# Optimization experiments

Hardware: AMD Instinct MI355X
Metric: run time of the kernel (lower is better)

The kernel has to match this reference:

```python
import jax, jax.numpy as jnp
import numpy as np

B, D, E, H, A = 4096, 1024, 8, 1024, 512  # batch, state_dim, num_options, num_neurons, num_actions


def setup_inputs() -> dict:
    key = jax.random.key(0)
    ks = jax.random.split(key, 16)
    s = 0.02
    return {
        "state": jax.random.normal(ks[0], (B, D), jnp.float32),
        "selected_options": jax.random.randint(ks[1], (B,), 0, E, jnp.int32),
        # option network: Linear(D,H) -> ReLU -> Linear(H,E)
        "Wo1": jax.random.normal(ks[2], (D, H), jnp.float32) * s,
        "bo1": jnp.zeros((H,), jnp.float32),
        "Wo2": jax.random.normal(ks[3], (H, E), jnp.float32) * s,
        "bo2": jnp.zeros((E,), jnp.float32),
        # E expert nets, each: Linear(D,H)+ReLU -> Linear(H,H)+ReLU -> Linear(H,A)
        "We1": jax.random.normal(ks[4], (E, D, H), jnp.float32) * s,
        "be1": jnp.zeros((E, H), jnp.float32),
        "We2": jax.random.normal(ks[5], (E, H, H), jnp.float32) * s,
        "be2": jnp.zeros((E, H), jnp.float32),
        "We3": jax.random.normal(ks[6], (E, H, A), jnp.float32) * s,
        "be3": jnp.zeros((E, A), jnp.float32),
        # termination network: Linear(D,H) -> ReLU -> Linear(H,1) -> Sigmoid
        "Wt1": jax.random.normal(ks[7], (D, H), jnp.float32) * s,
        "bt1": jnp.zeros((H,), jnp.float32),
        "Wt2": jax.random.normal(ks[8], (H, 1), jnp.float32) * s,
        "bt2": jnp.zeros((1,), jnp.float32),
    }


def reference(state, selected_options, Wo1, bo1, Wo2, bo2,
              We1, be1, We2, be2, We3, be3, Wt1, bt1, Wt2, bt2):
    # option head
    option_probs = jax.nn.softmax(jnp.maximum(state @ Wo1 + bo1, 0.0) @ Wo2 + bo2, axis=-1)

    # expert MLPs: compute all experts vectorized, then gather per-sample selected expert.
    # (the torch code loops per sample; equal action sizes so no padding is needed)
    h = jnp.maximum(jnp.einsum("bd,edh->beh", state, We1) + be1, 0.0)   # [B,E,H]
    h = jnp.maximum(jnp.einsum("beh,ehk->bek", h, We2) + be2, 0.0)      # [B,E,H]
    logits = jnp.einsum("beh,eha->bea", h, We3) + be3                   # [B,E,A]
    probs_all = jax.nn.softmax(logits, axis=-1)
    sel = selected_options[:, None, None]
    action_probs = jnp.take_along_axis(probs_all, sel, axis=1)[:, 0, :]  # [B,A]
    selected_actions = jnp.argmax(action_probs, axis=-1)

    # termination head
    termination_prob = jax.nn.sigmoid(jnp.maximum(state @ Wt1 + bt1, 0.0) @ Wt2 + bt2)

    return option_probs, action_probs, termination_prob, selected_options, selected_actions
```

## Files before the change

kernel.cpp:

```cpp
#include <hip/hip_runtime.h>
#include <hip/hip_bf16.h>

#define B_ 4096
#define D_ 1024
#define E_ 8
#define H_ 1024
#define A_ 512
#define PB 6144
#define NTT 24
#define FB_CAP 128
#define FROWS (E_ * FB_CAP)
#define KSPLIT 4
#define MARGIN 3.0e-3f

typedef __attribute__((ext_vector_type(8))) short s16x8;
typedef __attribute__((ext_vector_type(4))) float f32x4;

__device__ __forceinline__ unsigned short f2bf(float f) {
    __hip_bfloat16 h = __float2bfloat16(f);
    return *reinterpret_cast<unsigned short*>(&h);
}
__device__ __forceinline__ float bf2f(unsigned short u) {
    return __uint_as_float(((unsigned int)u) << 16);
}
__device__ __forceinline__ void gload16(const void* g, void* l) {
    __builtin_amdgcn_global_load_lds(
        (const __attribute__((address_space(1))) unsigned int*)g,
        (__attribute__((address_space(3))) unsigned int*)l, 16, 0, 0);
}

__device__ __forceinline__ int a_src_chunk(int lane) { return (((lane & 7) ^ (lane >> 3)) * 8); }

__device__ __forceinline__ int t32idx(int k, int c2) {
    return k * 64 + ((c2 + 5 * (k >> 3) + k) & 63);
}

__device__ __forceinline__ void tr_tile_128x128(const float* __restrict__ src, int Nsrc,
                                                unsigned short* __restrict__ dst,
                                                unsigned int* T32) {
    const int t = threadIdx.x;
#pragma unroll
    for (int i = 0; i < 16; ++i) {
        const int id = t + i * 256;
        const int r  = id >> 5;
        const int c4 = (id & 31) * 4;
        const float4 v = *(const float4*)&src[(size_t)r * Nsrc + c4];
        const unsigned int u0 = (unsigned)f2bf(v.x) | ((unsigned)f2bf(v.y) << 16);
        const unsigned int u1 = (unsigned)f2bf(v.z) | ((unsigned)f2bf(v.w) << 16);
        T32[t32idx(r, (c4 >> 1) + 0)] = u0;
        T32[t32idx(r, (c4 >> 1) + 1)] = u1;
    }
    __syncthreads();
#pragma unroll
    for (int q = 0; q < 8; ++q) {
        const int id = t + q * 256;
        const int n = id >> 4;
        const int L = id & 15;
        const int hi = n & 1;
        unsigned int w[4];
#pragma unroll
        for (int jj = 0; jj < 4; ++jj) {
            const int k0 = L * 8 + 2 * jj;
            const unsigned int a = T32[t32idx(k0,     n >> 1)];
            const unsigned int b = T32[t32idx(k0 + 1, n >> 1)];
            const unsigned int ha = hi ? (a >> 16) : (a & 0xffffu);
            const unsigned int hb = hi ? (b >> 16) : (b & 0xffffu);
            w[jj] = ha | (hb << 16);
        }
        *(uint4*)&dst[(size_t)n * 1024 + L * 8] = make_uint4(w[0], w[1], w[2], w[3]);
    }
}

__global__ __launch_bounds__(256)
void k_prep(const float* __restrict__ x, unsigned short* __restrict__ y,
            const float* __restrict__ Wo1, const float* __restrict__ Wt1,
            unsigned short* __restrict__ Wbf,
            const float* __restrict__ We1, unsigned short* __restrict__ We1t,
            const float* __restrict__ We2, unsigned short* __restrict__ We2t,
            const float* __restrict__ We3, unsigned short* __restrict__ We3t,
            const int* __restrict__ sel, int* __restrict__ tile_expert,
            int* __restrict__ rowlist, int* __restrict__ pos_of_row,
            int* __restrict__ rowlist2, int* __restrict__ cur2) {
    __shared__ unsigned int T32[128 * 64];
    const int t = threadIdx.x;
    const int bid = blockIdx.x;
    if (bid >= 2177) {
        const int q = bid - 2177;
        const int e = q >> 5, r = q & 31, kt = r >> 2, ntb = r & 3;
        tr_tile_128x128(We3 + (size_t)e * 524288 + (size_t)(kt * 128) * 512 + ntb * 128, 512,
                        We3t + (size_t)e * 524288 + (size_t)(ntb * 128) * 1024 + kt * 128, T32);
        return;
    }
    if (bid >= 1665) {
        const int q = bid - 1665;
        const int e = q >> 6, r = q & 63, kt = r >> 3, ntb = r & 7;
        tr_tile_128x128(We2 + (size_t)e * 1048576 + (size_t)(kt * 128) * 1024 + ntb * 128, 1024,
                        We2t + (size_t)e * 1048576 + (size_t)(ntb * 128) * 1024 + kt * 128, T32);
        return;
    }
    if (bid >= 1153) {
        const int q = bid - 1153;
        const int e = q >> 6, r = q & 63, kt = r >> 3, ntb = r & 7;
        tr_tile_128x128(We1 + (size_t)e * 1048576 + (size_t)(kt * 128) * 1024 + ntb * 128, 1024,
                        We1t + (size_t)e * 1048576 + (size_t)(ntb * 128) * 1024 + kt * 128, T32);
        return;
    }
    if (bid >= 1025) {
        const int q = bid - 1025;
        const int m = q >> 6, r = q & 63, kt = r >> 3, ntb = r & 7;
        const float* src = (m ? Wt1 : Wo1) + (size_t)(kt * 128) * 1024 + ntb * 128;
        tr_tile_128x128(src, 1024,
                        Wbf + (size_t)(m * 1024 + ntb * 128) * 1024 + kt * 128, T32);
        return;
    }
    if (bid > 0) {
        const int base = (bid - 1) * 1024 + t;
#pragma unroll
        for (int j = 0; j < 4; ++j) {
            const int i = base + j * 256;
            float4 v = ((const float4*)x)[i];
            ushort4 o;
            o.x = f2bf(v.x); o.y = f2bf(v.y); o.z = f2bf(v.z); o.w = f2bf(v.w);
            ((ushort4*)y)[i] = o;
        }
        return;
    }
    __shared__ int scnt[E_], soff[E_], scur[E_];
    if (t < E_) { scnt[t] = 0; scur[t] = 0; cur2[t] = 0; }
    for (int i = t; i < PB; i += 256) rowlist[i] = -1;
    for (int i = t; i < FROWS; i += 256) rowlist2[i] = -1;
    __syncthreads();
    for (int b = t; b < B_; b += 256) {
        int e = sel[b]; e = e < 0 ? 0 : (e >= E_ ? E_ - 1 : e);
        atomicAdd(&scnt[e], 1);
    }
    __syncthreads();
    if (t == 0) {
        int off = 0;
        for (int e = 0; e < E_; ++e) {
            soff[e] = off;
            int tiles = (scnt[e] + 255) >> 8;
            for (int k = 0; k < tiles; ++k) tile_expert[(off >> 8) + k] = e;
            off += tiles << 8;
        }
        for (int k = off >> 8; k < NTT; ++k) tile_expert[k] = -1;
    }
    __syncthreads();
    for (int b = t; b < B_; b += 256) {
        int e = sel[b]; e = e < 0 ? 0 : (e >= E_ ? E_ - 1 : e);
        int pos = atomicAdd(&scur[e], 1);
        int p = soff[e] + pos; if (p >= PB) p = PB - 1;
        rowlist[p] = b;
        pos_of_row[b] = p;
    }
}

template<int TN>
__device__ __forceinline__ void gemm3(
    const unsigned short* __restrict__ g0, const unsigned short* __restrict__ g1,
    const unsigned short* __restrict__ g2, const unsigned short* __restrict__ g3,
    const unsigned short* __restrict__ Bt, int Kg, const float* __restrict__ bp,
    unsigned short* __restrict__ Cbf, float* __restrict__ Cf, int Ncols, int relu,
    unsigned short* As, unsigned short* Bs)
{
    constexpr int NI = TN / 32;
    constexpr int BTH = TN * 64;
    constexpr int BR = TN / 64;
    constexpr int LPT = 4 + BR;
    const int t = threadIdx.x, lane = t & 63, w = t >> 6;
    const int wr = w >> 1, wc = w & 1;
    const int aseg = w * 2048 + lane * 8;
    const int bseg = w * (BR * 512) + lane * 8;
    const int coffb = a_src_chunk(lane);
    const unsigned short* bsrc = Bt + (size_t)(w * BR * 8 + (lane >> 3)) * Kg + coffb;

    f32x4 acc[4][NI];
#pragma unroll
    for (int i = 0; i < 4; ++i)
#pragma unroll
        for (int j = 0; j < NI; ++j)
#pragma unroll
            for (int r = 0; r < 4; ++r) acc[i][j][r] = 0.f;

#define G_STAGE(IT, BUF) {                                                   \
        const int ko_ = (IT) * 64;                                           \
        const int oa_ = (BUF) * 16384 + aseg;                                \
        gload16(g0 + ko_, As + oa_);                                         \
        gload16(g1 + ko_, As + oa_ + 512);                                   \
        gload16(g2 + ko_, As + oa_ + 1024);                                  \
        gload16(g3 + ko_, As + oa_ + 1536);                                  \
        const int ob_ = (BUF) * BTH + bseg;                                  \
        _Pragma("unroll")                                                    \
        for (int j_ = 0; j_ < BR; ++j_)                                      \
            gload16(bsrc + ko_ + (size_t)(j_ * 8) * Kg, Bs + ob_ + j_ * 512); \
    }

    G_STAGE(0, 0);

    for (int it = 0; it < 16; ++it) {
        const int cb = it & 1;
        if (it + 1 < 16) {
            G_STAGE(it + 1, cb ^ 1);
            if constexpr (LPT == 8)      asm volatile("s_waitcnt vmcnt(8)" ::: "memory");
            else if constexpr (LPT == 6) asm volatile("s_waitcnt vmcnt(6)" ::: "memory");
            else                         asm volatile("s_waitcnt vmcnt(5)" ::: "memory");
        } else {
            asm volatile("s_waitcnt vmcnt(0)" ::: "memory");
        }
        __builtin_amdgcn_s_barrier();
        __builtin_amdgcn_sched_barrier(0);
        __builtin_amdgcn_s_setprio(1);
#pragma unroll
        for (int kq = 0; kq < 2; ++kq) {
            const int sc = kq * 4 + (lane >> 4);
            s16x8 af[4], bfr[NI];
#pragma unroll
            for (int mi = 0; mi < 4; ++mi) {
                const int ar = wr * 64 + mi * 16 + (lane & 15);
                af[mi] = *reinterpret_cast<const s16x8*>(
                    &As[cb * 16384 + ar * 64 + ((sc ^ (ar & 7)) << 3)]);
            }
#pragma unroll
            for (int ni = 0; ni < NI; ++ni) {
                const int br = wc * (TN / 2) + ni * 16 + (lane & 15);
                bfr[ni] = *reinterpret_cast<const s16x8*>(
                    &Bs[cb * BTH + br * 64 + ((sc ^ (br & 7)) << 3)]);
            }
#pragma unroll
            for (int mi = 0; mi < 4; ++mi)
#pragma unroll
                for (int ni = 0; ni < NI; ++ni)
                    acc[mi][ni] = __builtin_amdgcn_mfma_f32_16x16x32_bf16(
                        af[mi], bfr[ni], acc[mi][ni], 0, 0, 0);
        }
        __builtin_amdgcn_s_setprio(0);
        if (it + 1 < 16) {
            asm volatile("s_waitcnt lgkmcnt(0)" ::: "memory");
            __builtin_amdgcn_sched_barrier(0);
            __builtin_amdgcn_s_barrier();
        }
    }
#undef G_STAGE

    const int cq = lane >> 4, cr = lane & 15;
#pragma unroll
    for (int ni = 0; ni < NI; ++ni) {
        const int col_l = wc * (TN / 2) + ni * 16 + cr;
        const float bv = bp[col_l];
#pragma unroll
        for (int mi = 0; mi < 4; ++mi) {
#pragma unroll
            for (int r = 0; r < 4; ++r) {
                const int row_l = wr * 64 + mi * 16 + cq * 4 + r;
                float v = acc[mi][ni][r] + bv;
                if (relu) v = fmaxf(v, 0.f);
                const size_t idx = (size_t)row_l * Ncols + col_l;
                if (Cbf) Cbf[idx] = f2bf(v);
                if (Cf)  Cf[idx] = v;
            }
        }
    }
}

__global__ __launch_bounds__(512, 2)
void k_d2(const unsigned short* __restrict__ Sbf,
          const int* __restrict__ rowlist, const int* __restrict__ tile_expert,
          const unsigned short* __restrict__ Wbf,
          const float* __restrict__ bo1, const float* __restrict__ bt1,
          const unsigned short* __restrict__ We1t, const float* __restrict__ be1,
          unsigned short* __restrict__ hopt, unsigned short* __restrict__ hterm,
          unsigned short* __restrict__ h1) {
    __shared__ __align__(16) unsigned short SMEM[4 * 16384];
    unsigned short* As = SMEM;
    unsigned short* Bs = SMEM + 2 * 16384;
    const int bid = blockIdx.x;
    const int t = threadIdx.x, lane = t & 63, w = t >> 6;
    const int coff = a_src_chunk(lane);
    const int r0l = w * 32 + (lane >> 3);
    if (bid < 128) {
        const int nt = bid & 7, mt = bid >> 3;
        const unsigned short* g0 = Sbf + (size_t)(mt * 256 + r0l) * D_ + coff;
        const unsigned short* g1 = g0 + (size_t)8 * D_;
        const unsigned short* g2 = g0 + (size_t)16 * D_;
        const unsigned short* g3 = g0 + (size_t)24 * D_;
        int ntRow; const float* bp; unsigned short* C;
        if (nt < 4) { ntRow = nt * 256; bp = bo1 + nt * 256;
                      C = hopt + (size_t)(mt * 256) * H_ + nt * 256; }
        else { ntRow = 1024 + (nt - 4) * 256; bp = bt1 + (nt - 4) * 256;
               C = hterm + (size_t)(mt * 256) * H_ + (nt - 4) * 256; }
        gemm3<256>(g0, g1, g2, g3, Wbf + (size_t)ntRow * 1024, 1024, bp,
                   C, nullptr, H_, 1, As, Bs);
    } else {
        const int q = bid - 128, nt = q & 3, mt = q >> 2;
        const int e = tile_expert[mt]; if (e < 0) return;
        const int base = mt * 256;
        const int sub = rowlist[base]; if (sub < 0) return;
        int r0 = rowlist[base + r0l];      if (r0 < 0) r0 = sub;
        int r1 = rowlist[base + r0l + 8];  if (r1 < 0) r1 = sub;
        int r2 = rowlist[base + r0l + 16]; if (r2 < 0) r2 = sub;
        int r3 = rowlist[base + r0l + 24]; if (r3 < 0) r3 = sub;
        const unsigned short* g0 = Sbf + (size_t)r0 * D_ + coff;
        const unsigned short* g1 = Sbf + (size_t)r1 * D_ + coff;
        const unsigned short* g2 = Sbf + (size_t)r2 * D_ + coff;
        const unsigned short* g3 = Sbf + (size_t)r3 * D_ + coff;
        gemm3<256>(g0, g1, g2, g3,
                   We1t + (size_t)e * 1048576 + (size_t)(nt * 256) * 1024, 1024,
                   be1 + (size_t)e * H_ + nt * 256,
                   h1 + (size_t)(mt * 256) * H_ + nt * 256, nullptr, H_, 1, As, Bs);
    }
}

__global__ __launch_bounds__(512, 2)
void k_d3(const unsigned short* __restrict__ h1, const int* __restrict__ tile_expert,
          const unsigned short* __restrict__ We2t, const float* __restrict__ be2,
          unsigned short* __restrict__ h2) {
    __shared__ __align__(16) unsigned short SMEM[2 * 16384 + 2 * 8192];
    unsigned short* As = SMEM;
    unsigned short* Bs = SMEM + 2 * 16384;
    const int t = threadIdx.x, lane = t & 63, w = t >> 6;
    const int coff = a_src_chunk(lane);
    const int r0l = w * 32 + (lane >> 3);
    const int nt = blockIdx.x & 7, mt = blockIdx.x >> 3;
    const int e = tile_expert[mt]; if (e < 0) return;
    const unsigned short* g0 = h1 + (size_t)(mt * 256 + r0l) * H_ + coff;
    gemm3<128>(g0, g0 + (size_t)8 * H_, g0 + (size_t)16 * H_, g0 + (size_t)24 * H_,
               We2t + (size_t)e * 1048576 + (size_t)(nt * 128) * 1024, 1024,
               be2 + (size_t)e * H_ + nt * 128,
               h2 + (size_t)(mt * 256) * H_ + nt * 128, nullptr, H_, 1, As, Bs);
}

__global__ __launch_bounds__(512, 2)
void k_d5(const unsigned short* __restrict__ h2, const int* __restrict__ tile_expert,
          const unsigned short* __restrict__ We3t, const float* __restrict__ be3,
          float* __restrict__ lgt) {
    __shared__ __align__(16) unsigned short SMEM[2 * 16384 + 2 * 4096];
    unsigned short* As = SMEM;
    unsigned short* Bs = SMEM + 2 * 16384;
    const int t = threadIdx.x, lane = t & 63, w = t >> 6;
    const int coff = a_src_chunk(lane);
    const int r0l = w * 32 + (lane >> 3);
    const int nt = blockIdx.x & 7, mt = blockIdx.x >> 3;
    const int e = tile_expert[mt]; if (e < 0) return;
    const unsigned short* g0 = h2 + (size_t)(mt * 256 + r0l) * H_ + coff;
    gemm3<64>(g0, g0 + (size_t)8 * H_, g0 + (size_t)16 * H_, g0 + (size_t)24 * H_,
              We3t + (size_t)e * 524288 + (size_t)(nt * 64) * 1024, 1024,
              be3 + (size_t)e * A_ + nt * 64,
              nullptr, lgt + (size_t)(mt * 256) * A_ + nt * 64, A_, 0, As, Bs);
}

__device__ __forceinline__ void opt_body(int b, const unsigned short* __restrict__ h,
                                         const float* __restrict__ Wo2, const float* __restrict__ bo2,
                                         float* __restrict__ out, float* sm) {
    const int t = threadIdx.x;
    float acc[E_];
#pragma unroll
    for (int j = 0; j < E_; ++j) acc[j] = 0.f;
    for (int k = t; k < H_; k += 256) {
        float hv = bf2f(h[(size_t)b * H_ + k]);
#pragma unroll
        for (int j = 0; j < E_; ++j) acc[j] = fmaf(hv, Wo2[k * E_ + j], acc[j]);
    }
#pragma unroll
    for (int j = 0; j < E_; ++j)
        for (int off = 32; off; off >>= 1) acc[j] += __shfl_down(acc[j], off, 64);
    float* red = sm;
    float* probs = sm + 4 * E_;
    int wave = t >> 6, lane = t & 63;
    if (lane == 0)
        for (int j = 0; j < E_; ++j) red[wave * E_ + j] = acc[j];
    __syncthreads();
    if (t == 0) {
        float z[E_]; float m = -1e30f;
        for (int j = 0; j < E_; ++j) {
            z[j] = red[j] + red[E_ + j] + red[2 * E_ + j] + red[3 * E_ + j] + bo2[j];
            m = fmaxf(m, z[j]);
        }
        float s = 0.f;
        for (int j = 0; j < E_; ++j) { z[j] = expf(z[j] - m); s += z[j]; }
        float inv = 1.f / s;
        for (int j = 0; j < E_; ++j) probs[j] = z[j] * inv;
    }
    __syncthreads();
    if (t < E_) out[(size_t)b * E_ + t] = probs[t];
}

__device__ __forceinline__ void term_body(int b, const unsigned short* __restrict__ h,
                                          const float* __restrict__ Wt2, const float* __restrict__ bt2,
                                          float* __restrict__ out, float* sm) {
    const int t = threadIdx.x;
    float acc = 0.f;
    for (int k = t; k < H_; k += 256) acc = fmaf(bf2f(h[(size_t)b * H_ + k]), Wt2[k], acc);
    for (int off = 32; off; off >>= 1) acc += __shfl_down(acc, off, 64);
    if ((t & 63) == 0) sm[t >> 6] = acc;
    __syncthreads();
    if (t == 0) {
        float z = sm[0] + sm[1] + sm[2] + sm[3] + bt2[0];
        out[b] = 1.f / (1.f + expf(-z));
    }
}

__global__ __launch_bounds__(256)
void k_gather(const float* __restrict__ logits, const int* __restrict__ pos_of_row,
              const int* __restrict__ sel,
              float* __restrict__ out_probs, float* __restrict__ out_selopt,
              float* __restrict__ out_selact,
              int* __restrict__ rowlist2, int* __restrict__ cur2,
              const unsigned short* __restrict__ hopt, const float* __restrict__ Wo2,
              const float* __restrict__ bo2, float* __restrict__ out_opt,
              const unsigned short* __restrict__ hterm, const float* __restrict__ Wt2,
              const float* __restrict__ bt2, float* __restrict__ out_term) {
    __shared__ float smbuf[5 * E_ + 8];
    const int bid = blockIdx.x;
    if (bid >= 2 * B_) { term_body(bid - 2 * B_, hterm, Wt2, bt2, out_term, smbuf); return; }
    if (bid >= B_)     { opt_body(bid - B_, hopt, Wo2, bo2, out_opt, smbuf); return; }

    const int b = bid;
    int p = pos_of_row[b];
    if (p < 0) p = 0; if (p >= PB) p = PB - 1;
    const int t = threadIdx.x;
    const float* L = logits + (size_t)p * A_;
    float v0 = L[t], v1 = L[t + 256];

    float bv; int bi;
    if (v0 >= v1) { bv = v0; bi = t; } else { bv = v1; bi = t + 256; }
    for (int off = 32; off; off >>= 1) {
        float ov = __shfl_down(bv, off, 64);
        int   oi = __shfl_down(bi, off, 64);
        if (ov > bv || (ov == bv && oi < bi)) { bv = ov; bi = oi; }
    }
    __shared__ float rv[4]; __shared__ int ri[4];
    int wave = t >> 6, lane = t & 63;
    if (lane == 0) { rv[wave] = bv; ri[wave] = bi; }
    __syncthreads();
    __shared__ float sM; __shared__ int sBi;
    if (t == 0) {
        float mv = rv[0]; int mi = ri[0];
        for (int w = 1; w < 4; ++w)
            if (rv[w] > mv || (rv[w] == mv && ri[w] < mi)) { mv = rv[w]; mi = ri[w]; }
        sM = mv; sBi = mi;
    }
    __syncthreads();
    const float M = sM; const int BI = sBi;

    float e0 = expf(v0 - M), e1 = expf(v1 - M);
    float s = e0 + e1;
    for (int off = 32; off; off >>= 1) s += __shfl_down(s, off, 64);
    __shared__ float reds[4];
    if (lane == 0) reds[wave] = s;
    __syncthreads();
    float inv = 1.f / (reds[0] + reds[1] + reds[2] + reds[3]);

    out_probs[(size_t)b * A_ + t]       = e0 * inv;
    out_probs[(size_t)b * A_ + t + 256] = e1 * inv;

    float s0 = (t == BI) ? -1e30f : v0;
    float s1 = (t + 256 == BI) ? -1e30f : v1;
    float sm = fmaxf(s0, s1);
    for (int off = 32; off; off >>= 1) sm = fmaxf(sm, __shfl_down(sm, off, 64));
    __shared__ float red2[4];
    if (lane == 0) red2[wave] = sm;
    __syncthreads();

    if (t == 0) {
        float second = fmaxf(fmaxf(red2[0], red2[1]), fmaxf(red2[2], red2[3]));
        out_selact[b] = (float)BI;
        int e = sel[b]; e = e < 0 ? 0 : (e >= E_ ? E_ - 1 : e);
        out_selopt[b] = (float)sel[b];
        if (M - second < MARGIN) {
            int pos = atomicAdd(&cur2[e], 1);
            if (pos < FB_CAP) rowlist2[e * FB_CAP + pos] = b;
        }
    }
}

#define BM 64
#define BN 64
#define BK 32

__global__ __launch_bounds__(256)
void k_pgemm(const float* __restrict__ A, int lda, const int* __restrict__ flags,
             int gather, const float* __restrict__ W,
             float* __restrict__ P, int K, int N) {
    __shared__ float As_[BK][BM + 4];
    __shared__ float Bs_[BK][BN];

    const int mt = blockIdx.y, nt = blockIdx.x, kz = blockIdx.z;
    if (flags[mt * BM] < 0) return;
    const int e = mt >> 1;
    const float* Wb = W + (size_t)e * K * N + (size_t)nt * BN;

    const int t  = threadIdx.x;
    const int tx = t & 15;
    const int ty = t >> 4;

    const int arow = t >> 3;
    const int ak   = (t & 7) * 4;
    int r0 = mt * BM + arow, r1 = r0 + 32;
    if (gather) { r0 = flags[r0]; r1 = flags[r1]; }
    const int bkr = t >> 4;
    const int bn  = (t & 15) * 4;

    float acc[4][4];
#pragma unroll
    for (int i = 0; i < 4; ++i)
#pragma unroll
        for (int j = 0; j < 4; ++j) acc[i][j] = 0.0f;

    const int kbeg = kz * (K / KSPLIT);
    const int kend = kbeg + (K / KSPLIT);
    for (int k0 = kbeg; k0 < kend; k0 += BK) {
        float4 a0 = make_float4(0.f, 0.f, 0.f, 0.f), a1 = a0;
        if (r0 >= 0) a0 = *(const float4*)&A[(size_t)r0 * lda + k0 + ak];
        if (r1 >= 0) a1 = *(const float4*)&A[(size_t)r1 * lda + k0 + ak];
        float4 b0 = *(const float4*)&Wb[(size_t)(k0 + bkr) * N + bn];
        float4 b1 = *(const float4*)&Wb[(size_t)(k0 + bkr + 16) * N + bn];

        __syncthreads();
        As_[ak + 0][arow] = a0.x; As_[ak + 1][arow] = a0.y;
        As_[ak + 2][arow] = a0.z; As_[ak + 3][arow] = a0.w;
        As_[ak + 0][arow + 32] = a1.x; As_[ak + 1][arow + 32] = a1.y;
        As_[ak + 2][arow + 32] = a1.z; As_[ak + 3][arow + 32] = a1.w;
        *(float4*)&Bs_[bkr][bn]      = b0;
        *(float4*)&Bs_[bkr + 16][bn] = b1;
        __syncthreads();

#pragma unroll
        for (int kk = 0; kk < BK; ++kk) {
            const float4 av = *(const float4*)&As_[kk][ty * 4];
            const float4 bv = *(const float4*)&Bs_[kk][tx * 4];
            const float a_[4] = {av.x, av.y, av.z, av.w};
            const float b_[4] = {bv.x, bv.y, bv.z, bv.w};
#pragma unroll
            for (int i = 0; i < 4; ++i)
#pragma unroll
                for (int j = 0; j < 4; ++j)
                    acc[i][j] = fmaf(a_[i], b_[j], acc[i][j]);
        }
    }

    float* Pz = P + (size_t)kz * FROWS * N;
    const int n0 = nt * BN + tx * 4;
#pragma unroll
    for (int i = 0; i < 4; ++i) {
        int m = mt * BM + ty * 4 + i;
        *(float4*)&Pz[(size_t)m * N + n0] = make_float4(acc[i][0], acc[i][1], acc[i][2], acc[i][3]);
    }
}

__global__ __launch_bounds__(256)
void k_fred(const float* __restrict__ P, const int* __restrict__ flags,
            const float* __restrict__ bias, float* __restrict__ C, int N, int relu) {
    const int m = blockIdx.x;
    if (flags[m] < 0) return;
    const int e = m >> 7;
    const int t = threadIdx.x;
    if (t * 4 >= N) return;
    const size_t MN = (size_t)FROWS * N;
    const size_t base = (size_t)m * N + t * 4;
    float4 s = *(const float4*)&P[base];
#pragma unroll
    for (int z = 1; z < KSPLIT; ++z) {
        float4 p = *(const float4*)&P[(size_t)z * MN + base];
        s.x += p.x; s.y += p.y; s.z += p.z; s.w += p.w;
    }
    const float* bp = bias + (size_t)e * N + t * 4;
    s.x += bp[0]; s.y += bp[1]; s.z += bp[2]; s.w += bp[3];
    if (relu) {
        s.x = fmaxf(s.x, 0.f); s.y = fmaxf(s.y, 0.f);
        s.z = fmaxf(s.z, 0.f); s.w = fmaxf(s.w, 0.f);
    }
    *(float4*)&C[base] = s;
}

__global__ __launch_bounds__(256)
void k_fixup(const float* __restrict__ logitsf, const int* __restrict__ rowlist2,
             float* __restrict__ out_probs, float* __restrict__ out_selact) {
    const int i = blockIdx.x;
    const int row = rowlist2[i];
    if (row < 0) return;
    const int t = threadIdx.x;
    const float* L = logitsf + (size_t)i * A_;
    float v0 = L[t], v1 = L[t + 256];

    float bv; int bi;
    if (v0 >= v1) { bv = v0; bi = t; } else { bv = v1; bi = t + 256; }
    for (int off = 32; off; off >>= 1) {
        float ov = __shfl_down(bv, off, 64);
        int   oi = __shfl_down(bi, off, 64);
        if (ov > bv || (ov == bv && oi < bi)) { bv = ov; bi = oi; }
    }
    __shared__ float rv[4]; __shared__ int ri[4];
    int wave = t >> 6, lane = t & 63;
    if (lane == 0) { rv[wave] = bv; ri[wave] = bi; }
    __syncthreads();
    __shared__ float sM; __shared__ int sBi;
    if (t == 0) {
        float mv = rv[0]; int mi = ri[0];
        for (int w = 1; w < 4; ++w)
            if (rv[w] > mv || (rv[w] == mv && ri[w] < mi)) { mv = rv[w]; mi = ri[w]; }
        sM = mv; sBi = mi;
    }
    __syncthreads();

    float e0 = expf(v0 - sM), e1 = expf(v1 - sM);
    float s = e0 + e1;
    for (int off = 32; off; off >>= 1) s += __shfl_down(s, off, 64);
    __shared__ float reds[4];
    if (lane == 0) reds[wave] = s;
    __syncthreads();
    float inv = 1.f / (reds[0] + reds[1] + reds[2] + reds[3]);

    out_probs[(size_t)row * A_ + t]       = e0 * inv;
    out_probs[(size_t)row * A_ + t + 256] = e1 * inv;
    if (t == 0) out_selact[row] = (float)sBi;
}

extern "C" void kernel_launch(void* const* d_in, const int* in_sizes, int n_in,
                              void* d_out, int out_size, void* d_ws, size_t ws_size,
                              hipStream_t stream) {
    const float* state = (const float*)d_in[0];
    const int*   sel   = (const int*)d_in[1];
    const float* Wo1 = (const float*)d_in[2];
    const float* bo1 = (const float*)d_in[3];
    const float* Wo2 = (const float*)d_in[4];
    const float* bo2 = (const float*)d_in[5];
    const float* We1 = (const float*)d_in[6];
    const float* be1 = (const float*)d_in[7];
    const float* We2 = (const float*)d_in[8];
    const float* be2 = (const float*)d_in[9];
    const float* We3 = (const float*)d_in[10];
    const float* be3 = (const float*)d_in[11];
    const float* Wt1 = (const float*)d_in[12];
    const float* bt1 = (const float*)d_in[13];
    const float* Wt2 = (const float*)d_in[14];
    const float* bt2 = (const float*)d_in[15];
    float* out = (float*)d_out;

    char* w = (char*)d_ws;
    int* meta        = (int*)w;
    int* rowlist     = meta;
    int* pos_of_row  = meta + 6144;
    int* rowlist2    = meta + 10240;
    int* tile_expert = meta + 11264;
    int* cur2        = meta + 11296;
    char* P0 = w + 65536;
    char* P1 = P0 + 12582912;
    char* P2 = P1 + 16777216;
    char* W1 = P2 + 12582912;
    char* W2 = W1 + 16777216;
    char* W3 = W2 + 16777216;
    unsigned short* Sbf   = (unsigned short*)P0;
    unsigned short* Wbf   = (unsigned short*)(P0 + (8u << 20));
    unsigned short* h2b   = (unsigned short*)P0;
    unsigned short* hopt  = (unsigned short*)P1;
    unsigned short* hterm = hopt + (size_t)B_ * H_;
    unsigned short* h1b   = (unsigned short*)P2;
    unsigned short* We1t  = (unsigned short*)W1;
    unsigned short* We2t  = (unsigned short*)W2;
    unsigned short* We3t  = (unsigned short*)W3;
    float* lgt  = (float*)P2;
    float* Pbuf = (float*)P1;
    float* h1f  = (float*)P0;
    float* h2f  = h1f + (size_t)FROWS * H_;
    float* lgf  = h2f + (size_t)FROWS * H_;

    size_t act_off    = (size_t)B_ * E_;
    size_t term_off   = act_off + (size_t)B_ * A_;
    size_t selopt_off = term_off + B_;
    size_t selact_off = selopt_off + B_;

    k_prep<<<2433, 256, 0, stream>>>(state, Sbf, Wo1, Wt1, Wbf, We1, We1t,
                                     We2, We2t, We3, We3t,
                                     sel, tile_expert, rowlist, pos_of_row, rowlist2, cur2);

    k_d2<<<224, 512, 0, stream>>>(Sbf, rowlist, tile_expert, Wbf,
                                  bo1, bt1, We1t, be1, hopt, hterm, h1b);
    k_d3<<<192, 512, 0, stream>>>(h1b, tile_expert, We2t, be2, h2b);
    k_d5<<<192, 512, 0, stream>>>(h2b, tile_expert, We3t, be3, lgt);

    k_gather<<<3 * B_, 256, 0, stream>>>(lgt, pos_of_row, sel,
                                         out + act_off, out + selopt_off, out + selact_off,
                                         rowlist2, cur2,
                                         hopt, Wo2, bo2, out,
                                         hterm, Wt2, bt2, out + term_off);

    k_pgemm<<<dim3(H_ / BN, FROWS / BM, KSPLIT), 256, 0, stream>>>(state, D_, rowlist2, 1, We1, Pbuf, D_, H_);
    k_fred<<<FROWS, 256, 0, stream>>>(Pbuf, rowlist2, be1, h1f, H_, 1);
    k_pgemm<<<dim3(H_ / BN, FROWS / BM, KSPLIT), 256, 0, stream>>>(h1f, H_, rowlist2, 0, We2, Pbuf, H_, H_);
    k_fred<<<FROWS, 256, 0, stream>>>(Pbuf, rowlist2, be2, h2f, H_, 1);
    k_pgemm<<<dim3(A_ / BN, FROWS / BM, KSPLIT), 256, 0, stream>>>(h2f, H_, rowlist2, 0, We3, Pbuf, H_, A_);
    k_fred<<<FROWS, 256, 0, stream>>>(Pbuf, rowlist2, be3, lgf, A_, 0);
    k_fixup<<<FROWS, 256, 0, stream>>>(lgf, rowlist2, out + act_off, out + selact_off);
}
```

Baseline: 214.5 us.

## Pad transposed bf16 weight rows and merge gather blocks into one per row

```diff
diff --git a/kernel.cpp b/kernel.cpp
--- a/kernel.cpp
+++ b/kernel.cpp
@@ -12,6 +12,7 @@
 #define FROWS (E_ * FB_CAP)
 #define KSPLIT 4
 #define MARGIN 3.0e-3f
+#define KGP 1056
 
 typedef __attribute__((ext_vector_type(8))) short s16x8;
 typedef __attribute__((ext_vector_type(4))) float f32x4;
@@ -36,7 +37,7 @@
 }
 
 __device__ __forceinline__ void tr_tile_128x128(const float* __restrict__ src, int Nsrc,
-                                                unsigned short* __restrict__ dst,
+                                                unsigned short* __restrict__ dst, int dstride,
                                                 unsigned int* T32) {
     const int t = threadIdx.x;
 #pragma unroll
@@ -67,7 +68,7 @@
             const unsigned int hb = hi ? (b >> 16) : (b & 0xffffu);
             w[jj] = ha | (hb << 16);
         }
-        *(uint4*)&dst[(size_t)n * 1024 + L * 8] = make_uint4(w[0], w[1], w[2], w[3]);
+        *(uint4*)&dst[(size_t)n * dstride + L * 8] = make_uint4(w[0], w[1], w[2], w[3]);
     }
 }
 
@@ -88,21 +89,24 @@
         const int q = bid - 2177;
         const int e = q >> 5, r = q & 31, kt = r >> 2, ntb = r & 3;
         tr_tile_128x128(We3 + (size_t)e * 524288 + (size_t)(kt * 128) * 512 + ntb * 128, 512,
-                        We3t + (size_t)e * 524288 + (size_t)(ntb * 128) * 1024 + kt * 128, T32);
+                        We3t + (size_t)e * 512 * KGP + (size_t)(ntb * 128) * KGP + kt * 128,
+                        KGP, T32);
         return;
     }
     if (bid >= 1665) {
         const int q = bid - 1665;
         const int e = q >> 6, r = q & 63, kt = r >> 3, ntb = r & 7;
         tr_tile_128x128(We2 + (size_t)e * 1048576 + (size_t)(kt * 128) * 1024 + ntb * 128, 1024,
-                        We2t + (size_t)e * 1048576 + (size_t)(ntb * 128) * 1024 + kt * 128, T32);
+                        We2t + (size_t)e * 1024 * KGP + (size_t)(ntb * 128) * KGP + kt * 128,
+                        KGP, T32);
         return;
     }
     if (bid >= 1153) {
         const int q = bid - 1153;
         const int e = q >> 6, r = q & 63, kt = r >> 3, ntb = r & 7;
         tr_tile_128x128(We1 + (size_t)e * 1048576 + (size_t)(kt * 128) * 1024 + ntb * 128, 1024,
-                        We1t + (size_t)e * 1048576 + (size_t)(ntb * 128) * 1024 + kt * 128, T32);
+                        We1t + (size_t)e * 1024 * KGP + (size_t)(ntb * 128) * KGP + kt * 128,
+                        KGP, T32);
         return;
     }
     if (bid >= 1025) {
@@ -110,7 +114,7 @@
         const int m = q >> 6, r = q & 63, kt = r >> 3, ntb = r & 7;
         const float* src = (m ? Wt1 : Wo1) + (size_t)(kt * 128) * 1024 + ntb * 128;
         tr_tile_128x128(src, 1024,
-                        Wbf + (size_t)(m * 1024 + ntb * 128) * 1024 + kt * 128, T32);
+                        Wbf + (size_t)(m * 1024 + ntb * 128) * KGP + kt * 128, KGP, T32);
         return;
     }
     if (bid > 0) {
@@ -288,7 +292,7 @@
                       C = hopt + (size_t)(mt * 256) * H_ + nt * 256; }
         else { ntRow = 1024 + (nt - 4) * 256; bp = bt1 + (nt - 4) * 256;
                C = hterm + (size_t)(mt * 256) * H_ + (nt - 4) * 256; }
-        gemm3<256>(g0, g1, g2, g3, Wbf + (size_t)ntRow * 1024, 1024, bp,
+        gemm3<256>(g0, g1, g2, g3, Wbf + (size_t)ntRow * KGP, KGP, bp,
                    C, nullptr, H_, 1, As, Bs);
     } else {
         const int q = bid - 128, nt = q & 3, mt = q >> 2;
@@ -304,7 +308,7 @@
         const unsigned short* g2 = Sbf + (size_t)r2 * D_ + coff;
         const unsigned short* g3 = Sbf + (size_t)r3 * D_ + coff;
         gemm3<256>(g0, g1, g2, g3,
-                   We1t + (size_t)e * 1048576 + (size_t)(nt * 256) * 1024, 1024,
+                   We1t + (size_t)e * 1024 * KGP + (size_t)(nt * 256) * KGP, KGP,
                    be1 + (size_t)e * H_ + nt * 256,
                    h1 + (size_t)(mt * 256) * H_ + nt * 256, nullptr, H_, 1, As, Bs);
     }
@@ -324,7 +328,7 @@
     const int e = tile_expert[mt]; if (e < 0) return;
     const unsigned short* g0 = h1 + (size_t)(mt * 256 + r0l) * H_ + coff;
     gemm3<128>(g0, g0 + (size_t)8 * H_, g0 + (size_t)16 * H_, g0 + (size_t)24 * H_,
-               We2t + (size_t)e * 1048576 + (size_t)(nt * 128) * 1024, 1024,
+               We2t + (size_t)e * 1024 * KGP + (size_t)(nt * 128) * KGP, KGP,
                be2 + (size_t)e * H_ + nt * 128,
                h2 + (size_t)(mt * 256) * H_ + nt * 128, nullptr, H_, 1, As, Bs);
 }
@@ -343,7 +347,7 @@
     const int e = tile_expert[mt]; if (e < 0) return;
     const unsigned short* g0 = h2 + (size_t)(mt * 256 + r0l) * H_ + coff;
     gemm3<64>(g0, g0 + (size_t)8 * H_, g0 + (size_t)16 * H_, g0 + (size_t)24 * H_,
-              We3t + (size_t)e * 524288 + (size_t)(nt * 64) * 1024, 1024,
+              We3t + (size_t)e * 512 * KGP + (size_t)(nt * 64) * KGP, KGP,
               be3 + (size_t)e * A_ + nt * 64,
               nullptr, lgt + (size_t)(mt * 256) * A_ + nt * 64, A_, 0, As, Bs);
 }
@@ -410,67 +414,73 @@
               const unsigned short* __restrict__ hterm, const float* __restrict__ Wt2,
               const float* __restrict__ bt2, float* __restrict__ out_term) {
     __shared__ float smbuf[5 * E_ + 8];
-    const int bid = blockIdx.x;
-    if (bid >= 2 * B_) { term_body(bid - 2 * B_, hterm, Wt2, bt2, out_term, smbuf); return; }
-    if (bid >= B_)     { opt_body(bid - B_, hopt, Wo2, bo2, out_opt, smbuf); return; }
-
-    const int b = bid;
-    int p = pos_of_row[b];
-    if (p < 0) p = 0; if (p >= PB) p = PB - 1;
+    __shared__ float smterm[8];
+    const int b = blockIdx.x;
     const int t = threadIdx.x;
-    const float* L = logits + (size_t)p * A_;
-    float v0 = L[t], v1 = L[t + 256];
-
-    float bv; int bi;
-    if (v0 >= v1) { bv = v0; bi = t; } else { bv = v1; bi = t + 256; }
-    for (int off = 32; off; off >>= 1) {
-        float ov = __shfl_down(bv, off, 64);
-        int   oi = __shfl_down(bi, off, 64);
-        if (ov > bv || (ov == bv && oi < bi)) { bv = ov; bi = oi; }
-    }
-    __shared__ float rv[4]; __shared__ int ri[4];
-    int wave = t >> 6, lane = t & 63;
-    if (lane == 0) { rv[wave] = bv; ri[wave] = bi; }
-    __syncthreads();
-    __shared__ float sM; __shared__ int sBi;
-    if (t == 0) {
-        float mv = rv[0]; int mi = ri[0];
-        for (int w = 1; w < 4; ++w)
-            if (rv[w] > mv || (rv[w] == mv && ri[w] < mi)) { mv = rv[w]; mi = ri[w]; }
-        sM = mv; sBi = mi;
-    }
-    __syncthreads();
-    const float M = sM; const int BI = sBi;
-
-    float e0 = expf(v0 - M), e1 = expf(v1 - M);
-    float s = e0 + e1;
-    for (int off = 32; off; off >>= 1) s += __shfl_down(s, off, 64);
-    __shared__ float reds[4];
-    if (lane == 0) reds[wave] = s;
-    __syncthreads();
-    float inv = 1.f / (reds[0] + reds[1] + reds[2] + reds[3]);
-
-    out_probs[(size_t)b * A_ + t]       = e0 * inv;
-    out_probs[(size_t)b * A_ + t + 256] = e1 * inv;
-
-    float s0 = (t == BI) ? -1e30f : v0;
-    float s1 = (t + 256 == BI) ? -1e30f : v1;
-    float sm = fmaxf(s0, s1);
-    for (int off = 32; off; off >>= 1) sm = fmaxf(sm, __shfl_down(sm, off, 64));
-    __shared__ float red2[4];
-    if (lane == 0) red2[wave] = sm;
-    __syncthreads();
-
-    if (t == 0) {
-        float second = fmaxf(fmaxf(red2[0], red2[1]), fmaxf(red2[2], red2[3]));
-        out_selact[b] = (float)BI;
-        int e = sel[b]; e = e < 0 ? 0 : (e >= E_ ? E_ - 1 : e);
-        out_selopt[b] = (float)sel[b];
-        if (M - second < MARGIN) {
-            int pos = atomicAdd(&cur2[e], 1);
-            if (pos < FB_CAP) rowlist2[e * FB_CAP + pos] = b;
-        }
-    }
+
+    {
+        int p = pos_of_row[b];
+        if (p < 0) p = 0; if (p >= PB) p = PB - 1;
+        const float* L = logits + (size_t)p * A_;
+        float v0 = L[t], v1 = L[t + 256];
+
+        float bv; int bi;
+        if (v0 >= v1) { bv = v0; bi = t; } else { bv = v1; bi = t + 256; }
+        for (int off = 32; off; off >>= 1) {
+            float ov = __shfl_down(bv, off, 64);
+            int   oi = __shfl_down(bi, off, 64);
+            if (ov > bv || (ov == bv && oi < bi)) { bv = ov; bi = oi; }
+        }
+        __shared__ float rv[4]; __shared__ int ri[4];
+        int wave = t >> 6, lane = t & 63;
+        if (lane == 0) { rv[wave] = bv; ri[wave] = bi; }
+        __syncthreads();
+        __shared__ float sM; __shared__ int sBi;
+        if (t == 0) {
+            float mv = rv[0]; int mi = ri[0];
+            for (int w = 1; w < 4; ++w)
+                if (rv[w] > mv || (rv[w] == mv && ri[w] < mi)) { mv = rv[w]; mi = ri[w]; }
+            sM = mv; sBi = mi;
+        }
+        __syncthreads();
+        const float M = sM; const int BI = sBi;
+
+        float e0 = expf(v0 - M), e1 = expf(v1 - M);
+        float s = e0 + e1;
+        for (int off = 32; off; off >>= 1) s += __shfl_down(s, off, 64);
+        __shared__ float reds[4];
+        if (lane == 0) reds[wave] = s;
+        __syncthreads();
+        float inv = 1.f / (reds[0] + reds[1] + reds[2] + reds[3]);
+
+        out_probs[(size_t)b * A_ + t]       = e0 * inv;
+        out_probs[(size_t)b * A_ + t + 256] = e1 * inv;
+
+        float s0 = (t == BI) ? -1e30f : v0;
+        float s1 = (t + 256 == BI) ? -1e30f : v1;
+        float sm = fmaxf(s0, s1);
+        for (int off = 32; off; off >>= 1) sm = fmaxf(sm, __shfl_down(sm, off, 64));
+        __shared__ float red2[4];
+        if (lane == 0) red2[wave] = sm;
+        __syncthreads();
+
+        if (t == 0) {
+            float second = fmaxf(fmaxf(red2[0], red2[1]), fmaxf(red2[2], red2[3]));
+            out_selact[b] = (float)BI;
+            int e = sel[b]; e = e < 0 ? 0 : (e >= E_ ? E_ - 1 : e);
+            out_selopt[b] = (float)sel[b];
+            if (M - second < MARGIN) {
+                int pos = atomicAdd(&cur2[e], 1);
+                if (pos < FB_CAP) rowlist2[e * FB_CAP + pos] = b;
+            }
+        }
+    }
+    __syncthreads();
+
+    opt_body(b, hopt, Wo2, bo2, out_opt, smbuf);
+    __syncthreads();
+
+    term_body(b, hterm, Wt2, bt2, out_term, smterm);
 }
 
 #define BM 64
@@ -644,11 +654,11 @@
     int* tile_expert = meta + 11264;
     int* cur2        = meta + 11296;
     char* P0 = w + 65536;
-    char* P1 = P0 + 12582912;
+    char* P1 = P0 + 12845056;
     char* P2 = P1 + 16777216;
     char* W1 = P2 + 12582912;
-    char* W2 = W1 + 16777216;
-    char* W3 = W2 + 16777216;
+    char* W2 = W1 + 17301504;
+    char* W3 = W2 + 17301504;
     unsigned short* Sbf   = (unsigned short*)P0;
     unsigned short* Wbf   = (unsigned short*)(P0 + (8u << 20));
     unsigned short* h2b   = (unsigned short*)P0;
@@ -678,11 +688,11 @@
     k_d3<<<192, 512, 0, stream>>>(h1b, tile_expert, We2t, be2, h2b);
     k_d5<<<192, 512, 0, stream>>>(h2b, tile_expert, We3t, be3, lgt);
 
-    k_gather<<<3 * B_, 256, 0, stream>>>(lgt, pos_of_row, sel,
-                                         out + act_off, out + selopt_off, out + selact_off,
-                                         rowlist2, cur2,
-                                         hopt, Wo2, bo2, out,
-                                         hterm, Wt2, bt2, out + term_off);
+    k_gather<<<B_, 256, 0, stream>>>(lgt, pos_of_row, sel,
+                                     out + act_off, out + selopt_off, out + selact_off,
+                                     rowlist2, cur2,
+                                     hopt, Wo2, bo2, out,
+                                     hterm, Wt2, bt2, out + term_off);
 
     k_pgemm<<<dim3(H_ / BN, FROWS / BM, KSPLIT), 256, 0, stream>>>(state, D_, rowlist2, 1, We1, Pbuf, D_, H_);
     k_fred<<<FROWS, 256, 0, stream>>>(Pbuf, rowlist2, be1, h1f, H_, 1);
```

New measurement: 218.5 us. No clear change (+1.9%).
